# Performance work log

Hardware: AMD Instinct MI355X
Metric: run time of the kernel (lower is better)

Reference implementation:

```python
import jax, jax.numpy as jnp
import numpy as np

NUM_LEVELS = 4
RADIUS = 4


def _bilinear_zeros(img, x, y):
    """Bilinear sample img (N,H,W) at absolute pixel coords x,y (N,S,S),
    zeros padding outside, matching torch grid_sample(align_corners=True,
    padding_mode='zeros') with absolute->normalized->absolute roundtrip."""
    N, H, W = img.shape
    x0 = jnp.floor(x); y0 = jnp.floor(y)
    x1 = x0 + 1.0;     y1 = y0 + 1.0
    wx1 = x - x0; wx0 = 1.0 - wx1
    wy1 = y - y0; wy0 = 1.0 - wy1
    flat = img.reshape(N, H * W)

    def gather(xi, yi):
        valid = (xi >= 0) & (xi <= W - 1) & (yi >= 0) & (yi <= H - 1)
        xc = jnp.clip(xi, 0, W - 1).astype(jnp.int32)
        yc = jnp.clip(yi, 0, H - 1).astype(jnp.int32)
        idx = (yc * W + xc).reshape(N, -1)
        v = jnp.take_along_axis(flat, idx, axis=1).reshape(xi.shape)
        return jnp.where(valid, v, jnp.zeros((), img.dtype))

    return (wy0 * wx0 * gather(x0, y0) + wy0 * wx1 * gather(x1, y0)
            + wy1 * wx0 * gather(x0, y1) + wy1 * wx1 * gather(x1, y1))


def _avg_pool2(v):
    N, H, W = v.shape
    return v.reshape(N, H // 2, 2, W // 2, 2).mean(axis=(2, 4))


def setup_inputs() -> dict:
    key = jax.random.key(0)
    k1, k2, k3 = jax.random.split(key, 3)
    B, M, C, H, W = 2, 4096, 256, 64, 64
    fmap1 = jax.random.normal(k1, (B, M, C), dtype=jnp.float32)
    fmap2 = jax.random.normal(k2, (B, C, H, W), dtype=jnp.float32)
    u = jax.random.uniform(k3, (B, M, 2), dtype=jnp.float32)
    centroids_coords = u * jnp.array([W - 1, H - 1], dtype=jnp.float32)
    return {"fmap1": fmap1, "fmap2": fmap2, "centroids_coords": centroids_coords}


def reference(fmap1, fmap2, centroids_coords):
    B, M, C = fmap1.shape
    _, _, H, W = fmap2.shape
    side = 2 * RADIUS + 1

    # correlation volume: (B, M, H, W) -> (B*M, H, W)
    corr = jnp.einsum('bmc,bchw->bmhw', fmap1, fmap2).reshape(B * M, H, W)

    d = jnp.arange(-RADIUS, RADIUS + 1, dtype=centroids_coords.dtype)
    di, dj = jnp.meshgrid(d, d, indexing='ij')
    delta = jnp.stack([di, dj], axis=-1)  # (S, S, 2): ch0 = x-offset, ch1 = y-offset

    c = centroids_coords.reshape(B * M, 1, 1, 2)
    vol = corr
    feats = []
    for lvl in range(NUM_LEVELS):
        sc = c + delta                        # (B*M, S, S, 2)
        sampled = _bilinear_zeros(vol, sc[..., 0], sc[..., 1])
        feats.append(sampled.reshape(B, M, side * side))
        c = c / 2.0
        if lvl < NUM_LEVELS - 1:
            vol = _avg_pool2(vol)
    # (B, M, num_levels*S*S) -> (B, out_channels, M)
    return jnp.concatenate(feats, axis=-1).transpose(0, 2, 1)
```

## Files before the change

kernel.cpp:

```cpp
#include <hip/hip_runtime.h>
#include <stdint.h>
#include <stddef.h>

static constexpr int Bb = 2;
static constexpr int Mq = 4096;
static constexpr int Cc = 256;
static constexpr int Hh = 64, Ww = 64;
static constexpr int Np = Hh * Ww;
static constexpr int RAD = 4;
static constexpr int SIDE = 2 * RAD + 1;
static constexpr int KPL = SIDE * SIDE;
static constexpr int NLVL = 4;
static constexpr int KTOT = NLVL * KPL;

typedef float floatx4 __attribute__((ext_vector_type(4)));
typedef short shortx8 __attribute__((ext_vector_type(8)));

union BfPack {
    shortx8 v;
    unsigned short u[8];
};

__device__ __forceinline__ unsigned short f2bf(float f) {
    unsigned int x = __float_as_uint(f);
    x += 0x7fffu + ((x >> 16) & 1u);
    return (unsigned short)(x >> 16);
}

__device__ __forceinline__ int ksw(int row, int g) {
    return 8 * (g ^ ((row >> 1) & 3));
}

__global__ __launch_bounds__(256)
void corr_gemm_kernel(const float* __restrict__ A,
                      const float* __restrict__ B2,
                      float* __restrict__ corr)
{
    __shared__ unsigned short la[128 * 32];
    __shared__ unsigned short lb[128 * 32];

    const int b    = blockIdx.z;
    const int bm0  = blockIdx.y * 128;
    const int bn0  = blockIdx.x * 128;
    const int tid  = threadIdx.x;
    const int lane = tid & 63;
    const int wave = tid >> 6;
    const int lane15 = lane & 15;
    const int quad   = lane >> 4;
    const int wm = (wave >> 1) * 64;
    const int wn = (wave & 1) * 64;

    const float* Abase = A + (size_t)(b * Mq + bm0) * Cc;
    const float* Bbase = B2 + (size_t)b * Cc * Np + bn0;

    floatx4 acc[4][4];
#pragma unroll
    for (int i = 0; i < 4; ++i)
#pragma unroll
        for (int j = 0; j < 4; ++j)
            acc[i][j] = floatx4{0.0f, 0.0f, 0.0f, 0.0f};

    const int a_row = tid >> 2;
    const int a_g   = tid & 3;
    const int b_n   = tid & 127;
    const int b_g0  = tid >> 7;

    for (int k0 = 0; k0 < Cc; k0 += 32) {
        __syncthreads();
#pragma unroll
        for (int r = 0; r < 2; ++r) {
            const int row = a_row + r * 64;
            const float* src = Abase + (size_t)row * Cc + k0 + a_g * 8;
            const float4 v0 = *(const float4*)(src);
            const float4 v1 = *(const float4*)(src + 4);
            BfPack p;
            p.u[0] = f2bf(v0.x); p.u[1] = f2bf(v0.y);
            p.u[2] = f2bf(v0.z); p.u[3] = f2bf(v0.w);
            p.u[4] = f2bf(v1.x); p.u[5] = f2bf(v1.y);
            p.u[6] = f2bf(v1.z); p.u[7] = f2bf(v1.w);
            *(shortx8*)&la[row * 32 + ksw(row, a_g)] = p.v;
        }
#pragma unroll
        for (int r = 0; r < 2; ++r) {
            const int g = b_g0 + r * 2;
            const float* src = Bbase + (size_t)(k0 + g * 8) * Np + b_n;
            BfPack p;
#pragma unroll
            for (int u = 0; u < 8; ++u)
                p.u[u] = f2bf(src[(size_t)u * Np]);
            *(shortx8*)&lb[b_n * 32 + ksw(b_n, g)] = p.v;
        }
        __syncthreads();
        shortx8 af[4], bf[4];
#pragma unroll
        for (int i = 0; i < 4; ++i) {
            const int row = wm + i * 16 + lane15;
            af[i] = *(const shortx8*)&la[row * 32 + ksw(row, quad)];
        }
#pragma unroll
        for (int j = 0; j < 4; ++j) {
            const int nn = wn + j * 16 + lane15;
            bf[j] = *(const shortx8*)&lb[nn * 32 + ksw(nn, quad)];
        }
#pragma unroll
        for (int i = 0; i < 4; ++i)
#pragma unroll
            for (int j = 0; j < 4; ++j)
                acc[i][j] = __builtin_amdgcn_mfma_f32_16x16x32_bf16(
                    af[i], bf[j], acc[i][j], 0, 0, 0);
    }

#pragma unroll
    for (int i = 0; i < 4; ++i) {
#pragma unroll
        for (int j = 0; j < 4; ++j) {
#pragma unroll
            for (int reg = 0; reg < 4; ++reg) {
                const int row = bm0 + wm + i * 16 + quad * 4 + reg;
                const int col = bn0 + wn + j * 16 + lane15;
                corr[(size_t)(b * Mq + row) * Np + col] = acc[i][j][reg];
            }
        }
    }
}

__global__ __launch_bounds__(256)
void pyr_sample_kernel(const float* __restrict__ cent,
                       const float* __restrict__ corr,
                       float* __restrict__ out)
{
    __shared__ float l1[8][1024];
    __shared__ float l2[8][256];
    __shared__ float l3[8][64];
    __shared__ float win0[8][100];
    __shared__ float qcx[8], qcy[8];
    __shared__ int   qx0[8], qy0[8];

    const int tid  = threadIdx.x;
    const int lane = tid & 63;
    const int wave = tid >> 6;
    const int b    = blockIdx.x >> 9;
    const int m0   = (blockIdx.x & 511) * 8;

    if (tid < 8) {
        const float cx = cent[(size_t)(b * Mq + m0 + tid) * 2 + 0];
        const float cy = cent[(size_t)(b * Mq + m0 + tid) * 2 + 1];
        qcx[tid] = cx; qcy[tid] = cy;
        qx0[tid] = (int)floorf(cx) - RAD;
        qy0[tid] = (int)floorf(cy) - RAD;
    }
    __syncthreads();

    const int xb = 4 * (lane & 15);
    const int rg = lane >> 4;
#pragma unroll
    for (int qi = 0; qi < 2; ++qi) {
        const int q = wave * 2 + qi;
        const float* src = corr + (size_t)(b * Mq + m0 + q) * Np;
        const int x0w = qx0[q], y0w = qy0[q];
#pragma unroll
        for (int it = 0; it < 16; ++it) {
            const float4 v = *(const float4*)(src + it * 256 + lane * 4);
            const int row = 4 * it + rg;
            float s0 = v.x + v.y;
            float s1 = v.z + v.w;
            s0 += __shfl_xor(s0, 16, 64);
            s1 += __shfl_xor(s1, 16, 64);
            if ((rg & 1) == 0) {
                const int r1 = row >> 1;
                const int c1 = 2 * (lane & 15);
                l1[q][r1 * 32 + c1]     = 0.25f * s0;
                l1[q][r1 * 32 + c1 + 1] = 0.25f * s1;
            }
            const int wy = row - y0w;
            if (wy >= 0 && wy < 10) {
                const float va[4] = {v.x, v.y, v.z, v.w};
#pragma unroll
                for (int u = 0; u < 4; ++u) {
                    const int wx = xb + u - x0w;
                    if (wx >= 0 && wx < 10) win0[q][wy * 10 + wx] = va[u];
                }
            }
        }
    }
    __syncthreads();

#pragma unroll
    for (int i = 0; i < 8; ++i) {
        const int idx = i * 256 + tid;
        const int q = idx >> 8;
        const int c = idx & 255;
        const int cy2 = c >> 4, cx2 = c & 15;
        const float* s = &l1[q][(2 * cy2) * 32 + 2 * cx2];
        l2[q][c] = 0.25f * (s[0] + s[1] + s[32] + s[33]);
    }
    __syncthreads();

#pragma unroll
    for (int i = 0; i < 2; ++i) {
        const int idx = i * 256 + tid;
        const int q = idx >> 6;
        const int c = idx & 63;
        const int cy3 = c >> 3, cx3 = c & 7;
        const float* s = &l2[q][(2 * cy3) * 16 + 2 * cx3];
        l3[q][c] = 0.25f * (s[0] + s[1] + s[16] + s[17]);
    }
    __syncthreads();

    for (int i = 0; i < 11; ++i) {
        const int idx = i * 256 + tid;
        if (idx >= KTOT * 8) break;
        const int q  = idx & 7;
        const int kk = idx >> 3;
        const int lvl = kk / KPL;
        const int r   = kk - lvl * KPL;
        const int di  = r / SIDE;
        const int dj  = r - di * SIDE;

        const int w = Ww >> lvl;
        const float scale = 1.0f / (float)(1 << lvl);
        const float x = qcx[q] * scale + (float)(di - RAD);
        const float y = qcy[q] * scale + (float)(dj - RAD);

        const float x0f = floorf(x), y0f = floorf(y);
        const float wx1 = x - x0f, wx0 = 1.0f - wx1;
        const float wy1 = y - y0f, wy0 = 1.0f - wy1;
        const float fmx = (float)(w - 1);
        const bool vx0 = (x0f >= 0.0f) && (x0f <= fmx);
        const bool vx1 = (x0f + 1.0f >= 0.0f) && (x0f + 1.0f <= fmx);
        const bool vy0 = (y0f >= 0.0f) && (y0f <= fmx);
        const bool vy1 = (y0f + 1.0f >= 0.0f) && (y0f + 1.0f <= fmx);

        const int ix0 = (int)x0f, iy0 = (int)y0f;

        const float* buf;
        int stride, ox, oy;
        if (lvl == 0)      { buf = win0[q]; stride = 10; ox = qx0[q]; oy = qy0[q]; }
        else if (lvl == 1) { buf = l1[q];   stride = 32; ox = 0; oy = 0; }
        else if (lvl == 2) { buf = l2[q];   stride = 16; ox = 0; oy = 0; }
        else               { buf = l3[q];   stride =  8; ox = 0; oy = 0; }

        const int cx0 = ix0 - ox, cx1 = ix0 + 1 - ox;
        const int cy0r = iy0 - oy, cy1r = iy0 + 1 - oy;
        const float g00 = (vx0 && vy0) ? buf[cy0r * stride + cx0] : 0.0f;
        const float g10 = (vx1 && vy0) ? buf[cy0r * stride + cx1] : 0.0f;
        const float g01 = (vx0 && vy1) ? buf[cy1r * stride + cx0] : 0.0f;
        const float g11 = (vx1 && vy1) ? buf[cy1r * stride + cx1] : 0.0f;

        out[((size_t)b * KTOT + kk) * Mq + m0 + q] =
            wy0 * (wx0 * g00 + wx1 * g10) + wy1 * (wx0 * g01 + wx1 * g11);
    }
}

extern "C" void kernel_launch(void* const* d_in, const int* in_sizes, int n_in,
                              void* d_out, int out_size, void* d_ws, size_t ws_size,
                              hipStream_t stream)
{
    const float* fmap1 = (const float*)d_in[0];
    const float* fmap2 = (const float*)d_in[1];
    const float* cent  = (const float*)d_in[2];
    float* corr = (float*)d_ws;
    float* out  = (float*)d_out;

    dim3 ggrid(Np / 128, Mq / 128, Bb);
    corr_gemm_kernel<<<ggrid, 256, 0, stream>>>(fmap1, fmap2, corr);

    const int nblk = Bb * Mq / 8;
    pyr_sample_kernel<<<nblk, 256, 0, stream>>>(cent, corr, out);
}
```

Measured before the change: 145.3 us.

## Fuse first pyramid pooling and window extraction into GEMM epilogue

The GEMM epilogue now stages each accumulator tile through shared memory and writes only the 2x2-pooled level-1 volume and the 10x10 level-0 window per query, instead of the full 64x64 correlation volume. The sampling kernel then loads these compact buffers rather than re-reading and pooling the full volume. This cuts global write and read traffic by about 4x. In exchange the GEMM gains extra shared memory and barriers, which may lower occupancy, and it relies on winbuf entries outside the image being ignored downstream.

```diff
diff --git a/kernel.cpp b/kernel.cpp
--- a/kernel.cpp
+++ b/kernel.cpp
@@ -13,6 +13,9 @@
 static constexpr int NLVL = 4;
 static constexpr int KTOT = NLVL * KPL;
 
+static constexpr size_t L1BUF_OFF  = 0;
+static constexpr size_t WINBUF_OFF = (size_t)Bb * Mq * 1024;
+
 typedef float floatx4 __attribute__((ext_vector_type(4)));
 typedef short shortx8 __attribute__((ext_vector_type(8)));
 
@@ -32,16 +35,21 @@
 }
 
 __global__ __launch_bounds__(256)
-void corr_gemm_kernel(const float* __restrict__ A,
-                      const float* __restrict__ B2,
-                      float* __restrict__ corr)
+void corr_gemm_pool_kernel(const float* __restrict__ A,
+                           const float* __restrict__ B2,
+                           const float* __restrict__ cent,
+                           float* __restrict__ l1buf,
+                           float* __restrict__ winbuf)
 {
     __shared__ unsigned short la[128 * 32];
     __shared__ unsigned short lb[128 * 32];
+    __shared__ float corrT[32 * 129];
+    __shared__ int   qx0s[128], qy0s[128];
 
     const int b    = blockIdx.z;
     const int bm0  = blockIdx.y * 128;
-    const int bn0  = blockIdx.x * 128;
+    const int bx   = blockIdx.x;
+    const int bn0  = bx * 128;
     const int tid  = threadIdx.x;
     const int lane = tid & 63;
     const int wave = tid >> 6;
@@ -49,6 +57,13 @@
     const int quad   = lane >> 4;
     const int wm = (wave >> 1) * 64;
     const int wn = (wave & 1) * 64;
+
+    if (tid < 128) {
+        const float cx = cent[(size_t)(b * Mq + bm0 + tid) * 2 + 0];
+        const float cy = cent[(size_t)(b * Mq + bm0 + tid) * 2 + 1];
+        qx0s[tid] = (int)floorf(cx) - RAD;
+        qy0s[tid] = (int)floorf(cy) - RAD;
+    }
 
     const float* Abase = A + (size_t)(b * Mq + bm0) * Cc;
     const float* Bbase = B2 + (size_t)b * Cc * Np + bn0;
@@ -110,15 +125,55 @@
                     af[i], bf[j], acc[i][j], 0, 0, 0);
     }
 
-#pragma unroll
-    for (int i = 0; i < 4; ++i) {
-#pragma unroll
-        for (int j = 0; j < 4; ++j) {
-#pragma unroll
-            for (int reg = 0; reg < 4; ++reg) {
-                const int row = bm0 + wm + i * 16 + quad * 4 + reg;
-                const int col = bn0 + wn + j * 16 + lane15;
-                corr[(size_t)(b * Mq + row) * Np + col] = acc[i][j][reg];
+    const int m_local = tid >> 3;
+    const int xi      = tid & 7;
+#pragma unroll
+    for (int c = 0; c < 4; ++c) {
+        __syncthreads();
+        if ((wave >> 1) == (c >> 1)) {
+#pragma unroll
+            for (int ii = 0; ii < 2; ++ii) {
+                const int i = 2 * (c & 1) + ii;
+#pragma unroll
+                for (int j = 0; j < 4; ++j) {
+#pragma unroll
+                    for (int reg = 0; reg < 4; ++reg) {
+                        const int rl = ii * 16 + quad * 4 + reg;
+                        const int n  = wn + j * 16 + lane15;
+                        corrT[rl * 129 + n] = acc[i][j][reg];
+                    }
+                }
+            }
+        }
+        __syncthreads();
+
+        const int mg = 32 * c + m_local;
+        const size_t gq = (size_t)(b * Mq + bm0 + mg);
+        const float* T = &corrT[m_local * 129];
+
+#pragma unroll
+        for (int k = 0; k < 4; ++k) {
+            const int c1 = xi + 8 * k;
+            const float v = 0.25f * (T[2 * c1] + T[2 * c1 + 1]
+                                   + T[64 + 2 * c1] + T[64 + 2 * c1 + 1]);
+            l1buf[gq * 1024 + bx * 32 + c1] = v;
+        }
+
+        const int x0w = qx0s[mg];
+        const int y0w = qy0s[mg];
+#pragma unroll
+        for (int par = 0; par < 2; ++par) {
+            const int wy = 2 * bx + par - y0w;
+            if (wy >= 0 && wy < 10) {
+#pragma unroll
+                for (int t = 0; t < 2; ++t) {
+                    const int wx = xi + t * 8;
+                    if (wx < 10) {
+                        const int x = x0w + wx;
+                        if (x >= 0 && x < Ww)
+                            winbuf[gq * 100 + wy * 10 + wx] = T[par * 64 + x];
+                    }
+                }
             }
         }
     }
@@ -126,7 +181,8 @@
 
 __global__ __launch_bounds__(256)
 void pyr_sample_kernel(const float* __restrict__ cent,
-                       const float* __restrict__ corr,
+                       const float* __restrict__ l1buf,
+                       const float* __restrict__ winbuf,
                        float* __restrict__ out)
 {
     __shared__ float l1[8][1024];
@@ -136,52 +192,30 @@
     __shared__ float qcx[8], qcy[8];
     __shared__ int   qx0[8], qy0[8];
 
-    const int tid  = threadIdx.x;
-    const int lane = tid & 63;
-    const int wave = tid >> 6;
-    const int b    = blockIdx.x >> 9;
-    const int m0   = (blockIdx.x & 511) * 8;
+    const int tid = threadIdx.x;
+    const int b   = blockIdx.x >> 9;
+    const int m0  = (blockIdx.x & 511) * 8;
+    const size_t gq0 = (size_t)(b * Mq + m0);
 
     if (tid < 8) {
-        const float cx = cent[(size_t)(b * Mq + m0 + tid) * 2 + 0];
-        const float cy = cent[(size_t)(b * Mq + m0 + tid) * 2 + 1];
+        const float cx = cent[(gq0 + tid) * 2 + 0];
+        const float cy = cent[(gq0 + tid) * 2 + 1];
         qcx[tid] = cx; qcy[tid] = cy;
         qx0[tid] = (int)floorf(cx) - RAD;
         qy0[tid] = (int)floorf(cy) - RAD;
     }
-    __syncthreads();
-
-    const int xb = 4 * (lane & 15);
-    const int rg = lane >> 4;
-#pragma unroll
-    for (int qi = 0; qi < 2; ++qi) {
-        const int q = wave * 2 + qi;
-        const float* src = corr + (size_t)(b * Mq + m0 + q) * Np;
-        const int x0w = qx0[q], y0w = qy0[q];
-#pragma unroll
-        for (int it = 0; it < 16; ++it) {
-            const float4 v = *(const float4*)(src + it * 256 + lane * 4);
-            const int row = 4 * it + rg;
-            float s0 = v.x + v.y;
-            float s1 = v.z + v.w;
-            s0 += __shfl_xor(s0, 16, 64);
-            s1 += __shfl_xor(s1, 16, 64);
-            if ((rg & 1) == 0) {
-                const int r1 = row >> 1;
-                const int c1 = 2 * (lane & 15);
-                l1[q][r1 * 32 + c1]     = 0.25f * s0;
-                l1[q][r1 * 32 + c1 + 1] = 0.25f * s1;
-            }
-            const int wy = row - y0w;
-            if (wy >= 0 && wy < 10) {
-                const float va[4] = {v.x, v.y, v.z, v.w};
-#pragma unroll
-                for (int u = 0; u < 4; ++u) {
-                    const int wx = xb + u - x0w;
-                    if (wx >= 0 && wx < 10) win0[q][wy * 10 + wx] = va[u];
-                }
-            }
-        }
+
+#pragma unroll
+    for (int it = 0; it < 8; ++it) {
+        const int v = it * 256 + tid;
+        const int q = v >> 8;
+        const int o = v & 255;
+        *(float4*)&l1[q][o * 4] = *(const float4*)&l1buf[(gq0 + q) * 1024 + o * 4];
+    }
+    if (tid < 200) {
+        const int q = tid / 25;
+        const int o = tid - q * 25;
+        *(float4*)&win0[q][o * 4] = *(const float4*)&winbuf[(gq0 + q) * 100 + o * 4];
     }
     __syncthreads();
 
@@ -195,7 +229,6 @@
         l2[q][c] = 0.25f * (s[0] + s[1] + s[32] + s[33]);
     }
     __syncthreads();
-
 #pragma unroll
     for (int i = 0; i < 2; ++i) {
         const int idx = i * 256 + tid;
@@ -259,12 +292,14 @@
     const float* fmap1 = (const float*)d_in[0];
     const float* fmap2 = (const float*)d_in[1];
     const float* cent  = (const float*)d_in[2];
-    float* corr = (float*)d_ws;
-    float* out  = (float*)d_out;
+    float* l1buf  = (float*)d_ws + L1BUF_OFF;
+    float* winbuf = (float*)d_ws + WINBUF_OFF;
+    float* out = (float*)d_out;
 
     dim3 ggrid(Np / 128, Mq / 128, Bb);
-    corr_gemm_kernel<<<ggrid, 256, 0, stream>>>(fmap1, fmap2, corr);
+    corr_gemm_pool_kernel<<<ggrid, 256, 0, stream>>>(fmap1, fmap2, cent,
+                                                     l1buf, winbuf);
 
     const int nblk = Bb * Mq / 8;
-    pyr_sample_kernel<<<nblk, 256, 0, stream>>>(cent, corr, out);
-}
+    pyr_sample_kernel<<<nblk, 256, 0, stream>>>(cent, l1buf, winbuf, out);
+}
```

New measurement: 129.0 us. 1.13x faster.
